# Optimization experiments

Measured on AMD Instinct MI355X. Metric: run time of the kernel, lower is better.

## Reference

```python
import jax, jax.numpy as jnp
import numpy as np

B, T, I, H = 64, 512, 1024, 1024

def setup_inputs() -> dict:
    key = jax.random.key(0)
    k1, k2, k3 = jax.random.split(key, 3)
    scale_x = 1.0 / np.sqrt(I)
    scale_h = 1.0 / np.sqrt(H)
    x = jax.random.normal(k1, (B, T, I), dtype=jnp.float32)
    Wx = jax.random.normal(k2, (I, 4 * H), dtype=jnp.float32) * scale_x
    Wh = jax.random.normal(k3, (H, 4 * H), dtype=jnp.float32) * scale_h
    b = jnp.zeros((4 * H,), dtype=jnp.float32)
    return {"x": x, "Wx": Wx, "Wh": Wh, "b": b}

def reference(x, Wx, Wh, b):
    # Standard LSTM over time: h_t, c_t carried; returns hidden sequence [B, T, H]
    Bq, Tq, _ = x.shape
    Hh = Wh.shape[0]
    # precompute input projections for all timesteps: [B, T, 4H]
    x_proj = jnp.einsum('bti,ig->btg', x, Wx) + b

    def step(carry, xp_t):
        h, c = carry
        gates = xp_t + h @ Wh  # [B, 4H]
        i, f, g, o = jnp.split(gates, 4, axis=-1)
        i = jax.nn.sigmoid(i)
        f = jax.nn.sigmoid(f)
        g = jnp.tanh(g)
        o = jax.nn.sigmoid(o)
        c_new = f * c + i * g
        h_new = o * jnp.tanh(c_new)
        return (h_new, c_new), h_new

    h0 = jnp.zeros((Bq, Hh), dtype=x.dtype)
    c0 = jnp.zeros((Bq, Hh), dtype=x.dtype)
    # scan over time axis
    (_, _), hs = jax.lax.scan(step, (h0, c0), jnp.swapaxes(x_proj, 0, 1))
    return jnp.swapaxes(hs, 0, 1)  # [B, T, H]
```

## Files before the change

kernel.cpp:

```cpp
#include <hip/hip_runtime.h>
#include <math.h>

#define Bq 64
#define Tq 512
#define Hq 1024
#define G4 4096
#define NBLK 256
#define NTHR 512

typedef __attribute__((ext_vector_type(8))) short short8;
typedef __attribute__((ext_vector_type(4))) float float4v;
typedef __attribute__((ext_vector_type(4))) unsigned uint4v;

static __device__ __forceinline__ short f2bf(float f) {
    union { float f; unsigned u; } c; c.f = f;
    unsigned r = (c.u + 0x7fffu + ((c.u >> 16) & 1u)) >> 16;
    return (short)r;
}

static __device__ __forceinline__ void astore_u(unsigned* p, unsigned v) {
    __hip_atomic_store(p, v, __ATOMIC_RELAXED, __HIP_MEMORY_SCOPE_AGENT);
}

static __device__ __forceinline__ float fsig(float v) {
    return 1.f / (1.f + __expf(-v));
}
static __device__ __forceinline__ float ftanh(float v) {
    float cl = fminf(fmaxf(v, -15.f), 15.f);
    float e  = __expf(-2.f * cl);
    return (1.f - e) / (1.f + e);
}

__global__ __launch_bounds__(NTHR, 1) void lstm_persist(
        const float* __restrict__ x, const float* __restrict__ Wx,
        const float* __restrict__ Wh, const float* __restrict__ bias,
        float* __restrict__ out, unsigned* __restrict__ hb0,
        unsigned* __restrict__ hb1)
{
    __shared__ float part[8][16][68];
    __shared__ float gtile[16][68];
    __shared__ float sbias[64];

    const int tid  = threadIdx.x;
    const int w    = tid >> 6;
    const int lane = tid & 63;
    const int blk  = blockIdx.x;
    const int mc   = blk & 3;
    const int jc   = blk >> 2;
    const int quad = lane >> 4;
    const int n    = lane & 15;
    const int gN   = n >> 2;
    const int jl4  = n & 3;

    if (tid < 64) {
        int u = tid >> 4, nn = tid & 15;
        sbias[u * 16 + nn] = bias[(nn >> 2) * Hq + jc * 16 + u * 4 + (nn & 3)];
    }

    short8 bs[4][8];
#pragma unroll
    for (int u = 0; u < 4; ++u) {
        const int col = gN * Hq + jc * 16 + u * 4 + jl4;
#pragma unroll
        for (int s = 0; s < 8; ++s) {
            const int kb = w * 128 + (s & 3) * 32 + quad * 8;
            const float* Wsrc = (s < 4) ? Wh : Wx;
#pragma unroll
            for (int j = 0; j < 8; ++j)
                bs[u][s][j] = f2bf(Wsrc[(size_t)(kb + j) * G4 + col]);
        }
    }

    float cstate = 0.f;
    const int urow = tid >> 4;
    const int ujl  = tid & 15;

    const int m_g = mc * 16 + n;
    const float* xrow = x + (size_t)m_g * Tq * Hq + w * 128 + quad * 8;
    const size_t hoff = (size_t)m_g * Hq + w * 128 + quad * 8;

    float4v acc0, acc1, acc2, acc3;

    auto mfma_chunk = [&](short8 a, int s) {
        acc0 = __builtin_amdgcn_mfma_f32_16x16x32_bf16(a, bs[0][s], acc0, 0, 0, 0);
        acc1 = __builtin_amdgcn_mfma_f32_16x16x32_bf16(a, bs[1][s], acc1, 0, 0, 0);
        acc2 = __builtin_amdgcn_mfma_f32_16x16x32_bf16(a, bs[2][s], acc2, 0, 0, 0);
        acc3 = __builtin_amdgcn_mfma_f32_16x16x32_bf16(a, bs[3][s], acc3, 0, 0, 0);
    };
    auto store_part = [&]() {
#pragma unroll
        for (int r = 0; r < 4; ++r) {
            part[w][quad * 4 + r][ 0 + n] = acc0[r];
            part[w][quad * 4 + r][16 + n] = acc1[r];
            part[w][quad * 4 + r][32 + n] = acc2[r];
            part[w][quad * 4 + r][48 + n] = acc3[r];
        }
    };
    auto xmfma = [&](const float4* xv) {
#pragma unroll
        for (int cs = 0; cs < 4; ++cs) {
            float4 v0 = xv[2 * cs], v1 = xv[2 * cs + 1];
            short8 a;
            a[0] = f2bf(v0.x); a[1] = f2bf(v0.y); a[2] = f2bf(v0.z); a[3] = f2bf(v0.w);
            a[4] = f2bf(v1.x); a[5] = f2bf(v1.y); a[6] = f2bf(v1.z); a[7] = f2bf(v1.w);
            mfma_chunk(a, 4 + cs);
        }
    };

    auto poll_h = [&](int t) {
        const unsigned* hb = (t & 1) ? hb1 : hb0;
        const unsigned* base = hb + hoff;
        const unsigned tg = (unsigned)t;
        uint4v q0, q1, q2, q3, q4, q5, q6, q7;
        for (;;) {
            asm volatile(
                "global_load_dwordx4 %[a0], %[ad], off sc0 sc1\n\t"
                "global_load_dwordx4 %[a1], %[ad], off offset:16 sc0 sc1\n\t"
                "global_load_dwordx4 %[a2], %[ad], off offset:128 sc0 sc1\n\t"
                "global_load_dwordx4 %[a3], %[ad], off offset:144 sc0 sc1\n\t"
                "global_load_dwordx4 %[a4], %[ad], off offset:256 sc0 sc1\n\t"
                "global_load_dwordx4 %[a5], %[ad], off offset:272 sc0 sc1\n\t"
                "global_load_dwordx4 %[a6], %[ad], off offset:384 sc0 sc1\n\t"
                "global_load_dwordx4 %[a7], %[ad], off offset:400 sc0 sc1\n\t"
                "s_waitcnt vmcnt(0)"
                : [a0]"=v"(q0), [a1]"=v"(q1), [a2]"=v"(q2), [a3]"=v"(q3),
                  [a4]"=v"(q4), [a5]"=v"(q5), [a6]"=v"(q6), [a7]"=v"(q7)
                : [ad]"v"(base)
                : "memory");
            unsigned bad = 0;
#pragma unroll
            for (int m = 0; m < 4; ++m) {
                bad |= (q0[m] ^ tg) & 0xffffu; bad |= (q1[m] ^ tg) & 0xffffu;
                bad |= (q2[m] ^ tg) & 0xffffu; bad |= (q3[m] ^ tg) & 0xffffu;
                bad |= (q4[m] ^ tg) & 0xffffu; bad |= (q5[m] ^ tg) & 0xffffu;
                bad |= (q6[m] ^ tg) & 0xffffu; bad |= (q7[m] ^ tg) & 0xffffu;
            }
            if (__all(bad == 0)) break;
        }
        auto mk = [&](uint4v qa, uint4v qb) {
            short8 a;
            a[0] = (short)(qa[0] >> 16); a[1] = (short)(qa[1] >> 16);
            a[2] = (short)(qa[2] >> 16); a[3] = (short)(qa[3] >> 16);
            a[4] = (short)(qb[0] >> 16); a[5] = (short)(qb[1] >> 16);
            a[6] = (short)(qb[2] >> 16); a[7] = (short)(qb[3] >> 16);
            return a;
        };
        mfma_chunk(mk(q0, q1), 0);
        mfma_chunk(mk(q2, q3), 1);
        mfma_chunk(mk(q4, q5), 2);
        mfma_chunk(mk(q6, q7), 3);
    };

    {
        float4 xv[8];
#pragma unroll
        for (int cs = 0; cs < 4; ++cs) {
            const float4* q = (const float4*)(xrow + cs * 32);
            xv[2 * cs] = q[0]; xv[2 * cs + 1] = q[1];
        }
        acc0 = acc1 = acc2 = acc3 = (float4v){0, 0, 0, 0};
        xmfma(xv);
        store_part();
    }

    for (int t = 0; t < Tq; ++t) {
        __syncthreads();
#pragma unroll
        for (int e = 0; e < 2; ++e) {
            int idx = tid + e * NTHR;
            int rr = idx >> 6, cc = idx & 63;
            float s = part[0][rr][cc];
#pragma unroll
            for (int ww = 1; ww < 8; ++ww) s += part[ww][rr][cc];
            gtile[rr][cc] = s + sbias[cc];
        }
        __syncthreads();

        const bool notlast = (t + 1 < Tq);

        float4 xv[8];
        if (notlast) {
            const float* ap = xrow + (size_t)(t + 1) * Hq;
#pragma unroll
            for (int cs = 0; cs < 4; ++cs) {
                const float4* q = (const float4*)(ap + cs * 32);
                xv[2 * cs] = q[0]; xv[2 * cs + 1] = q[1];
            }
        }

        if (tid < 256) {
            const int u = ujl >> 2, j4 = ujl & 3;
            float gi = gtile[urow][u * 16 +  0 + j4];
            float gf = gtile[urow][u * 16 +  4 + j4];
            float gg = gtile[urow][u * 16 +  8 + j4];
            float go = gtile[urow][u * 16 + 12 + j4];
            float i_ = fsig(gi);
            float f_ = fsig(gf);
            float g_ = ftanh(gg);
            float o_ = fsig(go);
            cstate = f_ * cstate + i_ * g_;
            float hn = o_ * ftanh(cstate);
            const int bg = mc * 16 + urow, jg = jc * 16 + ujl;
            if (notlast) {
                unsigned* hw = (t & 1) ? hb1 : hb0;
                astore_u(hw + (size_t)bg * Hq + jg,
                         ((unsigned)(unsigned short)f2bf(hn) << 16) | (unsigned)t);
            }
            out[((size_t)bg * Tq + t) * Hq + jg] = hn;
        }
        asm volatile("" ::: "memory");

        if (notlast) {
            acc0 = acc1 = acc2 = acc3 = (float4v){0, 0, 0, 0};
            xmfma(xv);
            poll_h(t);
            store_part();
        }
    }
}

extern "C" void kernel_launch(void* const* d_in, const int* in_sizes, int n_in,
                              void* d_out, int out_size, void* d_ws, size_t ws_size,
                              hipStream_t stream) {
    const float* x    = (const float*)d_in[0];
    const float* Wx   = (const float*)d_in[1];
    const float* Wh   = (const float*)d_in[2];
    const float* bias = (const float*)d_in[3];
    float* out = (float*)d_out;

    unsigned* hb0 = (unsigned*)d_ws;
    unsigned* hb1 = hb0 + Bq * Hq;

    hipMemsetAsync(d_ws, 0xFF, (size_t)2 * Bq * Hq * 4, stream);

    void* args[] = {(void*)&x, (void*)&Wx, (void*)&Wh, (void*)&bias,
                    (void*)&out, (void*)&hb0, (void*)&hb1};
    hipLaunchCooperativeKernel((const void*)lstm_persist, dim3(NBLK), dim3(NTHR),
                               args, 0, stream);
}
```

Measured before the change: 3.770 ms.

## Replace tagged per-element h polling with per-block flags and packed bf16 h

Hidden-state exchange between blocks changes from per-element 32-bit words carrying a step tag to bf16 values packed two per word. Readiness is now signalled by one flag per block, which consumers spin on before issuing a single h load. The next-step x loads are also issued before the gate reduction, and the output store is moved after the flag store. The aim is to cut polling traffic and the size of the h exchange. In exchange it adds an extra block barrier and a serial flag-then-load round trip each step, and relies on relaxed atomics with no explicit agent-scope release fence for ordering.

```diff
diff --git a/kernel.cpp b/kernel.cpp
--- a/kernel.cpp
+++ b/kernel.cpp
@@ -21,6 +21,9 @@
 static __device__ __forceinline__ void astore_u(unsigned* p, unsigned v) {
     __hip_atomic_store(p, v, __ATOMIC_RELAXED, __HIP_MEMORY_SCOPE_AGENT);
 }
+static __device__ __forceinline__ unsigned aload_u(const unsigned* p) {
+    return __hip_atomic_load(p, __ATOMIC_RELAXED, __HIP_MEMORY_SCOPE_AGENT);
+}
 
 static __device__ __forceinline__ float fsig(float v) {
     return 1.f / (1.f + __expf(-v));
@@ -34,8 +37,8 @@
 __global__ __launch_bounds__(NTHR, 1) void lstm_persist(
         const float* __restrict__ x, const float* __restrict__ Wx,
         const float* __restrict__ Wh, const float* __restrict__ bias,
-        float* __restrict__ out, unsigned* __restrict__ hb0,
-        unsigned* __restrict__ hb1)
+        float* __restrict__ out, unsigned* __restrict__ hp0,
+        unsigned* __restrict__ hp1, unsigned* __restrict__ flags)
 {
     __shared__ float part[8][16][68];
     __shared__ float gtile[16][68];
@@ -77,7 +80,7 @@
 
     const int m_g = mc * 16 + n;
     const float* xrow = x + (size_t)m_g * Tq * Hq + w * 128 + quad * 8;
-    const size_t hoff = (size_t)m_g * Hq + w * 128 + quad * 8;
+    const size_t hwoff = (size_t)m_g * (Hq / 2) + w * 64 + quad * 4;
 
     float4v acc0, acc1, acc2, acc3;
 
@@ -107,48 +110,40 @@
         }
     };
 
-    auto poll_h = [&](int t) {
-        const unsigned* hb = (t & 1) ? hb1 : hb0;
-        const unsigned* base = hb + hoff;
-        const unsigned tg = (unsigned)t;
-        uint4v q0, q1, q2, q3, q4, q5, q6, q7;
+    auto poll_flags = [&](unsigned tgt) {
+        const unsigned* fb = flags + mc * 64 + w * 8;
         for (;;) {
-            asm volatile(
-                "global_load_dwordx4 %[a0], %[ad], off sc0 sc1\n\t"
-                "global_load_dwordx4 %[a1], %[ad], off offset:16 sc0 sc1\n\t"
-                "global_load_dwordx4 %[a2], %[ad], off offset:128 sc0 sc1\n\t"
-                "global_load_dwordx4 %[a3], %[ad], off offset:144 sc0 sc1\n\t"
-                "global_load_dwordx4 %[a4], %[ad], off offset:256 sc0 sc1\n\t"
-                "global_load_dwordx4 %[a5], %[ad], off offset:272 sc0 sc1\n\t"
-                "global_load_dwordx4 %[a6], %[ad], off offset:384 sc0 sc1\n\t"
-                "global_load_dwordx4 %[a7], %[ad], off offset:400 sc0 sc1\n\t"
-                "s_waitcnt vmcnt(0)"
-                : [a0]"=v"(q0), [a1]"=v"(q1), [a2]"=v"(q2), [a3]"=v"(q3),
-                  [a4]"=v"(q4), [a5]"=v"(q5), [a6]"=v"(q6), [a7]"=v"(q7)
-                : [ad]"v"(base)
-                : "memory");
-            unsigned bad = 0;
+            unsigned f = aload_u(fb + (lane & 7));
+            if (__all((int)(f >= tgt))) break;
+        }
+    };
+
+    auto hload = [&](int t) {
+        const unsigned* hb = (t & 1) ? hp1 : hp0;
+        const unsigned* base = hb + hwoff;
+        uint4v q0, q1, q2, q3;
+        asm volatile(
+            "global_load_dwordx4 %[a0], %[ad], off sc0 sc1\n\t"
+            "global_load_dwordx4 %[a1], %[ad], off offset:64 sc0 sc1\n\t"
+            "global_load_dwordx4 %[a2], %[ad], off offset:128 sc0 sc1\n\t"
+            "global_load_dwordx4 %[a3], %[ad], off offset:192 sc0 sc1\n\t"
+            "s_waitcnt vmcnt(0)"
+            : [a0]"=v"(q0), [a1]"=v"(q1), [a2]"=v"(q2), [a3]"=v"(q3)
+            : [ad]"v"(base)
+            : "memory");
+        auto mk = [&](uint4v q) {
+            short8 a;
 #pragma unroll
             for (int m = 0; m < 4; ++m) {
-                bad |= (q0[m] ^ tg) & 0xffffu; bad |= (q1[m] ^ tg) & 0xffffu;
-                bad |= (q2[m] ^ tg) & 0xffffu; bad |= (q3[m] ^ tg) & 0xffffu;
-                bad |= (q4[m] ^ tg) & 0xffffu; bad |= (q5[m] ^ tg) & 0xffffu;
-                bad |= (q6[m] ^ tg) & 0xffffu; bad |= (q7[m] ^ tg) & 0xffffu;
+                a[2 * m]     = (short)(q[m] & 0xffffu);
+                a[2 * m + 1] = (short)(q[m] >> 16);
             }
-            if (__all(bad == 0)) break;
-        }
-        auto mk = [&](uint4v qa, uint4v qb) {
-            short8 a;
-            a[0] = (short)(qa[0] >> 16); a[1] = (short)(qa[1] >> 16);
-            a[2] = (short)(qa[2] >> 16); a[3] = (short)(qa[3] >> 16);
-            a[4] = (short)(qb[0] >> 16); a[5] = (short)(qb[1] >> 16);
-            a[6] = (short)(qb[2] >> 16); a[7] = (short)(qb[3] >> 16);
             return a;
         };
-        mfma_chunk(mk(q0, q1), 0);
-        mfma_chunk(mk(q2, q3), 1);
-        mfma_chunk(mk(q4, q5), 2);
-        mfma_chunk(mk(q6, q7), 3);
+        mfma_chunk(mk(q0), 0);
+        mfma_chunk(mk(q1), 1);
+        mfma_chunk(mk(q2), 2);
+        mfma_chunk(mk(q3), 3);
     };
 
     {
@@ -165,6 +160,19 @@
 
     for (int t = 0; t < Tq; ++t) {
         __syncthreads();
+
+        const bool notlast = (t + 1 < Tq);
+
+        float4 xv[8];
+        if (notlast) {
+            const float* ap = xrow + (size_t)(t + 1) * Hq;
+#pragma unroll
+            for (int cs = 0; cs < 4; ++cs) {
+                const float4* q = (const float4*)(ap + cs * 32);
+                xv[2 * cs] = q[0]; xv[2 * cs + 1] = q[1];
+            }
+        }
+
 #pragma unroll
         for (int e = 0; e < 2; ++e) {
             int idx = tid + e * NTHR;
@@ -176,18 +184,8 @@
         }
         __syncthreads();
 
-        const bool notlast = (t + 1 < Tq);
-
-        float4 xv[8];
-        if (notlast) {
-            const float* ap = xrow + (size_t)(t + 1) * Hq;
-#pragma unroll
-            for (int cs = 0; cs < 4; ++cs) {
-                const float4* q = (const float4*)(ap + cs * 32);
-                xv[2 * cs] = q[0]; xv[2 * cs + 1] = q[1];
-            }
-        }
-
+        float hn = 0.f;
+        int bg = 0, jg = 0;
         if (tid < 256) {
             const int u = ujl >> 2, j4 = ujl & 3;
             float gi = gtile[urow][u * 16 +  0 + j4];
@@ -199,21 +197,31 @@
             float g_ = ftanh(gg);
             float o_ = fsig(go);
             cstate = f_ * cstate + i_ * g_;
-            float hn = o_ * ftanh(cstate);
-            const int bg = mc * 16 + urow, jg = jc * 16 + ujl;
+            hn = o_ * ftanh(cstate);
+            bg = mc * 16 + urow;
+            jg = jc * 16 + ujl;
             if (notlast) {
-                unsigned* hw = (t & 1) ? hb1 : hb0;
-                astore_u(hw + (size_t)bg * Hq + jg,
-                         ((unsigned)(unsigned short)f2bf(hn) << 16) | (unsigned)t);
+                unsigned hp = (unsigned)(unsigned short)f2bf(hn);
+                unsigned up = __shfl_down(hp, 1);
+                if (!(tid & 1)) {
+                    unsigned* hw = (t & 1) ? hp1 : hp0;
+                    astore_u(hw + (size_t)bg * (Hq / 2) + (jg >> 1),
+                             hp | (up << 16));
+                }
             }
-            out[((size_t)bg * Tq + t) * Hq + jg] = hn;
-        }
+        }
+        __syncthreads();
+
+        if (notlast && tid == 0) astore_u(&flags[mc * 64 + jc], (unsigned)(t + 1));
         asm volatile("" ::: "memory");
+
+        if (tid < 256) out[((size_t)bg * Tq + t) * Hq + jg] = hn;
 
         if (notlast) {
             acc0 = acc1 = acc2 = acc3 = (float4v){0, 0, 0, 0};
             xmfma(xv);
-            poll_h(t);
+            poll_flags((unsigned)(t + 1));
+            hload(t);
             store_part();
         }
     }
@@ -228,13 +236,14 @@
     const float* bias = (const float*)d_in[3];
     float* out = (float*)d_out;
 
-    unsigned* hb0 = (unsigned*)d_ws;
-    unsigned* hb1 = hb0 + Bq * Hq;
-
-    hipMemsetAsync(d_ws, 0xFF, (size_t)2 * Bq * Hq * 4, stream);
+    unsigned* flags = (unsigned*)d_ws;
+    unsigned* hp0 = (unsigned*)((char*)d_ws + 1024);
+    unsigned* hp1 = hp0 + Bq * (Hq / 2);
+
+    hipMemsetAsync(d_ws, 0, 1024, stream);
 
     void* args[] = {(void*)&x, (void*)&Wx, (void*)&Wh, (void*)&bias,
-                    (void*)&out, (void*)&hb0, (void*)&hb1};
+                    (void*)&out, (void*)&hp0, (void*)&hp1, (void*)&flags};
     hipLaunchCooperativeKernel((const void*)lstm_persist, dim3(NBLK), dim3(NTHR),
                                args, 0, stream);
 }
```

After: 4.111 ms. 9.0% more time.
